# Kernel optimization log

Measured on AMD Instinct MI355X. Metric: run time of the kernel, lower is better.

## Reference

```python
import jax, jax.numpy as jnp
import numpy as np

N, E, IN, H = 100000, 400000, 128, 128
HEADS, HC = 4, 128  # GATConv(heads=4, out_channels=128, concat=False)
EPS = 1e-5


def setup_inputs() -> dict:
    key = jax.random.key(0)
    ks = jax.random.split(key, 16)
    rn = lambda i, shape, s=0.05: jax.random.normal(ks[i], shape, jnp.float32) * s
    return {
        "x": jax.random.normal(ks[0], (N, IN), jnp.float32),
        "edge_index": jax.random.randint(ks[1], (2, E), 0, N),
        # SAGEConv1: lin_l (aggregated neighbors, with bias) + lin_r (root)
        "Wl1": rn(2, (IN, H)), "Wr1": rn(3, (IN, H)), "b1": jnp.zeros((H,)),
        "g1": jnp.ones((H,)), "be1": jnp.zeros((H,)),
        # GATConv: shared lin, per-head attention vectors, bias (concat=False -> [HC])
        "Wg": rn(4, (H, HEADS * HC)), "att_s": rn(5, (HEADS, HC)), "att_d": rn(6, (HEADS, HC)), "bg": jnp.zeros((HC,)),
        "g2": jnp.ones((H,)), "be2": jnp.zeros((H,)),
        # SAGEConv3: hidden -> hidden//2
        "Wl3": rn(7, (H, H // 2)), "Wr3": rn(8, (H, H // 2)), "b3": jnp.zeros((H // 2,)),
        "g3": jnp.ones((H // 2,)), "be3": jnp.zeros((H // 2,)),
        # skip: in -> hidden//2
        "Wsk": rn(9, (IN, H // 2)), "bsk": jnp.zeros((H // 2,)),
        # classifier head: 64 -> 64 (BN+ReLU) -> 32 (ReLU) -> 2
        "Wc1": rn(10, (H // 2, 64)), "bc1": jnp.zeros((64,)),
        "gc": jnp.ones((64,)), "bec": jnp.zeros((64,)),
        "Wc2": rn(11, (64, 32)), "bc2": jnp.zeros((32,)),
        "Wc3": rn(12, (32, 2)), "bc3": jnp.zeros((2,)),
    }


def _bn(x, g, b):
    m = x.mean(0)
    v = x.var(0)
    return g * (x - m) * jax.lax.rsqrt(v + EPS) + b


def _sage(x, src, dst, Wl, Wr, b):
    # mean aggregation of neighbor features at dst, then lin_l(agg) + lin_r(x)
    agg = jax.ops.segment_sum(x[src], dst, num_segments=N)
    deg = jax.ops.segment_sum(jnp.ones((src.shape[0],), x.dtype), dst, num_segments=N)
    mean = agg / jnp.maximum(deg, 1.0)[:, None]
    return mean @ Wl + x @ Wr + b


def _gat(x, src, dst, Wg, att_s, att_d, bg):
    xh = (x @ Wg).reshape(N, HEADS, HC)          # [N,H,C]
    a_s = (xh * att_s).sum(-1)                    # [N,H]
    a_d = (xh * att_d).sum(-1)                    # [N,H]
    e = jax.nn.leaky_relu(a_s[src] + a_d[dst], 0.2)   # [E,H]
    emax = jax.lax.stop_gradient(jax.ops.segment_max(e, dst, num_segments=N))
    ee = jnp.exp(e - emax[dst])
    denom = jax.ops.segment_sum(ee, dst, num_segments=N)
    alpha = ee / jnp.maximum(denom, 1e-16)[dst]   # segment softmax over in-edges
    out = jax.ops.segment_sum(alpha[:, :, None] * xh[src], dst, num_segments=N)  # [N,H,C]
    return out.mean(1) + bg                       # concat=False -> mean over heads


def reference(x, edge_index, Wl1, Wr1, b1, g1, be1, Wg, att_s, att_d, bg, g2, be2,
              Wl3, Wr3, b3, g3, be3, Wsk, bsk, Wc1, bc1, gc, bec, Wc2, bc2, Wc3, bc3):
    src, dst = edge_index[0], edge_index[1]
    identity = x @ Wsk + bsk
    h = jax.nn.relu(_bn(_sage(x, src, dst, Wl1, Wr1, b1), g1, be1))
    h = jax.nn.relu(_bn(_gat(h, src, dst, Wg, att_s, att_d, bg), g2, be2))
    h = jax.nn.relu(_bn(_sage(h, src, dst, Wl3, Wr3, b3), g3, be3))
    emb = h + identity
    z = jax.nn.relu(_bn(emb @ Wc1 + bc1, gc, bec))
    z = jax.nn.relu(z @ Wc2 + bc2)
    return jax.nn.log_softmax(z @ Wc3 + bc3, axis=1)
```

## Files before the change

kernel.cpp:

```cpp
#include <hip/hip_runtime.h>
#include <hip/hip_bf16.h>
#include <cmath>


typedef short s16x8 __attribute__((ext_vector_type(8)));
typedef float f32x4 __attribute__((ext_vector_type(4)));

__device__ __forceinline__ float bf2f(unsigned short u) {
  return __uint_as_float((unsigned)u << 16);
}
__device__ __forceinline__ unsigned short f2bf(float f) {
  __hip_bfloat16 h = __float2bfloat16(f);
  return *reinterpret_cast<unsigned short*>(&h);
}

__global__ __launch_bounds__(256) void k_scan1(const int* __restrict__ cnt,
                                               int* __restrict__ bsum, int N) {
  int base = blockIdx.x << 10;
  int t = threadIdx.x;
  int s = 0;
  #pragma unroll
  for (int j = 0; j < 4; ++j) {
    int i = base + t * 4 + j;
    if (i < N) s += cnt[i];
  }
  __shared__ int red[256];
  red[t] = s;
  __syncthreads();
  for (int off = 128; off; off >>= 1) {
    if (t < off) red[t] += red[t + off];
    __syncthreads();
  }
  if (t == 0) bsum[blockIdx.x] = red[0];
}

__global__ __launch_bounds__(1024) void k_scan2(int* __restrict__ bsum, int nb) {
  __shared__ int sh[1024];
  int t = threadIdx.x;
  int v = (t < nb) ? bsum[t] : 0;
  sh[t] = v;
  __syncthreads();
  for (int off = 1; off < 1024; off <<= 1) {
    int u = (t >= off) ? sh[t - off] : 0;
    __syncthreads();
    sh[t] += u;
    __syncthreads();
  }
  if (t < nb) bsum[t] = sh[t] - v;
}

__global__ __launch_bounds__(256) void k_scan3(const int* __restrict__ cnt,
                                               const int* __restrict__ bsum,
                                               int* __restrict__ indptr,
                                               int* __restrict__ cursor, int N) {
  int base = blockIdx.x << 10;
  int t = threadIdx.x;
  int lane = t & 63, w = t >> 6;
  int i0 = base + t * 4;
  int v[4], s = 0;
  #pragma unroll
  for (int j = 0; j < 4; ++j) {
    int i = i0 + j;
    v[j] = (i < N) ? cnt[i] : 0;
    s += v[j];
  }
  int incl = s;
  #pragma unroll
  for (int off = 1; off < 64; off <<= 1) {
    int u = __shfl_up(incl, off);
    if (lane >= off) incl += u;
  }
  __shared__ int wsum[4];
  if (lane == 63) wsum[w] = incl;
  __syncthreads();
  int add = 0;
  for (int j = 0; j < w; ++j) add += wsum[j];
  int run = incl - s + add + bsum[blockIdx.x];
  #pragma unroll
  for (int j = 0; j < 4; ++j) {
    int i = i0 + j;
    if (i < N) {
      cursor[i] = run;
      run += v[j];
      indptr[i + 1] = run;
    }
  }
  if (blockIdx.x == 0 && t == 0) indptr[0] = 0;
}

__global__ void k_fill(const int* __restrict__ src, const int* __restrict__ dst,
                       int* __restrict__ cursor, int* __restrict__ csr_src, int E) {
  int e = blockIdx.x * blockDim.x + threadIdx.x;
  if (e >= E) return;
  int pos = atomicAdd(&cursor[dst[e]], 1);
  csr_src[pos] = src[e];
}

__global__ __launch_bounds__(256) void k_pre(
    const float* __restrict__ x, unsigned short* __restrict__ xbf, long n4,
    const int* __restrict__ dst, int* __restrict__ cnt, int E,
    int gC, int gE,
    const float* __restrict__ Wsk, const float* __restrict__ Wl1,
    const float* __restrict__ Wr1, const float* __restrict__ Wg,
    const float* __restrict__ Wl3, const float* __restrict__ Wr3,
    const float* __restrict__ Wc1, const float* __restrict__ Wc2,
    unsigned short* __restrict__ wt,
    const float* __restrict__ atts, const float* __restrict__ attd,
    float* __restrict__ attw) {
  int bx = blockIdx.x;
  if (bx < gC) {
    long t = (long)bx * 256 + threadIdx.x;
    if (t < n4) {
      float4 v = *reinterpret_cast<const float4*>(x + t * 4);
      ushort4 u;
      u.x = f2bf(v.x); u.y = f2bf(v.y); u.z = f2bf(v.z); u.w = f2bf(v.w);
      *reinterpret_cast<ushort4*>(xbf + t * 4) = u;
    }
    return;
  }
  bx -= gC;
  if (bx < gE) {
    int e = bx * 256 + threadIdx.x;
    if (e < E) atomicAdd(&cnt[dst[e]], 1);
    return;
  }
  bx -= gE;
  if (bx < 504) {
    int t = bx * 256 + threadIdx.x;
    if (t >= 129024) return;
    float v;
    if (t < 8192) {
      int c = t >> 7, k = t & 127;
      v = Wsk[k * 64 + c];
    } else if (t < 24576) {
      int r = t - 8192; int c = r >> 7, k = r & 127;
      v = Wl1[k * 128 + c];
    } else if (t < 40960) {
      int r = t - 24576; int c = r >> 7, k = r & 127;
      v = Wr1[k * 128 + c];
    } else if (t < 106496) {
      int r = t - 40960; int c = r >> 9; int q = r & 511; int h = q >> 7, k = q & 127;
      v = Wg[k * 512 + h * 128 + c];
    } else if (t < 114688) {
      int r = t - 106496; int c = r >> 7, k = r & 127;
      v = Wl3[k * 64 + c];
    } else if (t < 122880) {
      int r = t - 114688; int c = r >> 7, k = r & 127;
      v = Wr3[k * 64 + c];
    } else if (t < 126976) {
      int r = t - 122880; int c = r >> 6, k = r & 63;
      v = Wc1[k * 64 + c];
    } else {
      int r = t - 126976; int c = r >> 6, k = r & 63;
      v = Wc2[k * 32 + c];
    }
    wt[t] = f2bf(v);
    return;
  }
  bx -= 504;
  {
    int t = bx * 256 + threadIdx.x;
    if (t >= 1024) return;
    int k = t >> 3, j = t & 7, h = j & 3;
    const float* av = (j < 4 ? atts : attd) + h * 128;
    const float* wg = Wg + (size_t)k * 512 + h * 128;
    float s = 0.f;
    for (int c = 0; c < 128; ++c) s = fmaf(wg[c], av[c], s);
    attw[t] = s;
  }
}

__device__ __forceinline__ void gmean128_body(const unsigned short* __restrict__ X,
                                              const int* __restrict__ indptr,
                                              const int* __restrict__ csr,
                                              unsigned short* __restrict__ out,
                                              long wid, int lane) {
  int b = indptr[wid], en = indptr[wid + 1];
  float ax = 0.f, ay = 0.f;
  int i = b;
  for (; i + 3 < en; i += 4) {
    int s0 = csr[i], s1 = csr[i + 1], s2 = csr[i + 2], s3 = csr[i + 3];
    ushort2 u0 = *reinterpret_cast<const ushort2*>(X + ((size_t)s0 << 7) + (lane << 1));
    ushort2 u1 = *reinterpret_cast<const ushort2*>(X + ((size_t)s1 << 7) + (lane << 1));
    ushort2 u2 = *reinterpret_cast<const ushort2*>(X + ((size_t)s2 << 7) + (lane << 1));
    ushort2 u3 = *reinterpret_cast<const ushort2*>(X + ((size_t)s3 << 7) + (lane << 1));
    ax += bf2f(u0.x); ay += bf2f(u0.y);
    ax += bf2f(u1.x); ay += bf2f(u1.y);
    ax += bf2f(u2.x); ay += bf2f(u2.y);
    ax += bf2f(u3.x); ay += bf2f(u3.y);
  }
  for (; i < en; ++i) {
    int s = csr[i];
    ushort2 u = *reinterpret_cast<const ushort2*>(X + ((size_t)s << 7) + (lane << 1));
    ax += bf2f(u.x); ay += bf2f(u.y);
  }
  float inv = 1.0f / (float)max(en - b, 1);
  ax *= inv; ay *= inv;
  ushort2 o; o.x = f2bf(ax); o.y = f2bf(ay);
  *reinterpret_cast<ushort2*>(out + (wid << 7) + (lane << 1)) = o;
}

__global__ __launch_bounds__(256) void k_gmean64(const unsigned short* __restrict__ X,
                                                 const int* __restrict__ indptr,
                                                 const int* __restrict__ csr,
                                                 float* __restrict__ out, int N) {
  long wid = ((long)blockIdx.x * blockDim.x + threadIdx.x) >> 6;
  if (wid >= N) return;
  int lane = threadIdx.x & 63;
  int b = indptr[wid], en = indptr[wid + 1];
  float a = 0.f;
  int i = b;
  for (; i + 3 < en; i += 4) {
    int s0 = csr[i], s1 = csr[i + 1], s2 = csr[i + 2], s3 = csr[i + 3];
    unsigned short u0 = X[((size_t)s0 << 6) + lane];
    unsigned short u1 = X[((size_t)s1 << 6) + lane];
    unsigned short u2 = X[((size_t)s2 << 6) + lane];
    unsigned short u3 = X[((size_t)s3 << 6) + lane];
    a += bf2f(u0); a += bf2f(u1); a += bf2f(u2); a += bf2f(u3);
  }
  for (; i < en; ++i) {
    int s = csr[i];
    a += bf2f(X[((size_t)s << 6) + lane]);
  }
  out[(wid << 6) + lane] = a / (float)max(en - b, 1);
}

__global__ __launch_bounds__(256) void k_alpha(const int* __restrict__ indptr,
                                               const int* __restrict__ csr,
                                               const float* __restrict__ asad,
                                               float* __restrict__ alpha, int N) {
  long g = ((long)blockIdx.x * blockDim.x + threadIdx.x) >> 3;
  if (g >= N) return;
  int l8 = threadIdx.x & 7;
  int b = indptr[g], en = indptr[g + 1];
  float4 adv = *reinterpret_cast<const float4*>(asad + g * 8 + 4);
  float m[4] = {-INFINITY, -INFINITY, -INFINITY, -INFINITY};
  for (int i = b + l8; i < en; i += 8) {
    int s = csr[i];
    float4 a = *reinterpret_cast<const float4*>(asad + (size_t)s * 8);
    float e0 = a.x + adv.x, e1 = a.y + adv.y, e2 = a.z + adv.z, e3 = a.w + adv.w;
    e0 = e0 >= 0.f ? e0 : 0.2f * e0; e1 = e1 >= 0.f ? e1 : 0.2f * e1;
    e2 = e2 >= 0.f ? e2 : 0.2f * e2; e3 = e3 >= 0.f ? e3 : 0.2f * e3;
    m[0] = fmaxf(m[0], e0); m[1] = fmaxf(m[1], e1);
    m[2] = fmaxf(m[2], e2); m[3] = fmaxf(m[3], e3);
  }
  #pragma unroll
  for (int off = 1; off < 8; off <<= 1) {
    #pragma unroll
    for (int h = 0; h < 4; ++h) m[h] = fmaxf(m[h], __shfl_xor(m[h], off));
  }
  float den[4] = {0.f, 0.f, 0.f, 0.f};
  for (int i = b + l8; i < en; i += 8) {
    int s = csr[i];
    float4 a = *reinterpret_cast<const float4*>(asad + (size_t)s * 8);
    float e0 = a.x + adv.x, e1 = a.y + adv.y, e2 = a.z + adv.z, e3 = a.w + adv.w;
    e0 = e0 >= 0.f ? e0 : 0.2f * e0; e1 = e1 >= 0.f ? e1 : 0.2f * e1;
    e2 = e2 >= 0.f ? e2 : 0.2f * e2; e3 = e3 >= 0.f ? e3 : 0.2f * e3;
    float4 w;
    w.x = __expf(e0 - m[0]); w.y = __expf(e1 - m[1]);
    w.z = __expf(e2 - m[2]); w.w = __expf(e3 - m[3]);
    den[0] += w.x; den[1] += w.y; den[2] += w.z; den[3] += w.w;
    *reinterpret_cast<float4*>(alpha + (size_t)i * 4) = w;
  }
  #pragma unroll
  for (int off = 1; off < 8; off <<= 1) {
    #pragma unroll
    for (int h = 0; h < 4; ++h) den[h] += __shfl_xor(den[h], off);
  }
  float s0 = 0.25f / fmaxf(den[0], 1e-16f);
  float s1 = 0.25f / fmaxf(den[1], 1e-16f);
  float s2 = 0.25f / fmaxf(den[2], 1e-16f);
  float s3 = 0.25f / fmaxf(den[3], 1e-16f);
  for (int i = b + l8; i < en; i += 8) {
    float4 w = *reinterpret_cast<const float4*>(alpha + (size_t)i * 4);
    w.x *= s0; w.y *= s1; w.z *= s2; w.w *= s3;
    *reinterpret_cast<float4*>(alpha + (size_t)i * 4) = w;
  }
}

__global__ __launch_bounds__(256) void k_gath1(
    const unsigned short* __restrict__ h1, const int* __restrict__ indptr,
    const int* __restrict__ csr, const float* __restrict__ alpha,
    unsigned short* __restrict__ agg, int N) {
  long wid = ((long)blockIdx.x * blockDim.x + threadIdx.x) >> 6;
  if (wid >= N) return;
  int lane = threadIdx.x & 63;
  int b = indptr[wid], en = indptr[wid + 1];
  float a0x = 0.f, a0y = 0.f, a1x = 0.f, a1y = 0.f;
  float a2x = 0.f, a2y = 0.f, a3x = 0.f, a3y = 0.f;
  int i = b;
  for (; i + 3 < en; i += 4) {
    int s0 = csr[i], s1 = csr[i + 1], s2 = csr[i + 2], s3 = csr[i + 3];
    float4 A0 = *reinterpret_cast<const float4*>(alpha + (size_t)i * 4);
    float4 A1 = *reinterpret_cast<const float4*>(alpha + (size_t)(i + 1) * 4);
    float4 A2 = *reinterpret_cast<const float4*>(alpha + (size_t)(i + 2) * 4);
    float4 A3 = *reinterpret_cast<const float4*>(alpha + (size_t)(i + 3) * 4);
    ushort2 u0 = *reinterpret_cast<const ushort2*>(h1 + ((size_t)s0 << 7) + (lane << 1));
    ushort2 u1 = *reinterpret_cast<const ushort2*>(h1 + ((size_t)s1 << 7) + (lane << 1));
    ushort2 u2 = *reinterpret_cast<const ushort2*>(h1 + ((size_t)s2 << 7) + (lane << 1));
    ushort2 u3 = *reinterpret_cast<const ushort2*>(h1 + ((size_t)s3 << 7) + (lane << 1));
    float vx, vy;
    vx = bf2f(u0.x); vy = bf2f(u0.y);
    a0x = fmaf(A0.x, vx, a0x); a0y = fmaf(A0.x, vy, a0y);
    a1x = fmaf(A0.y, vx, a1x); a1y = fmaf(A0.y, vy, a1y);
    a2x = fmaf(A0.z, vx, a2x); a2y = fmaf(A0.z, vy, a2y);
    a3x = fmaf(A0.w, vx, a3x); a3y = fmaf(A0.w, vy, a3y);
    vx = bf2f(u1.x); vy = bf2f(u1.y);
    a0x = fmaf(A1.x, vx, a0x); a0y = fmaf(A1.x, vy, a0y);
    a1x = fmaf(A1.y, vx, a1x); a1y = fmaf(A1.y, vy, a1y);
    a2x = fmaf(A1.z, vx, a2x); a2y = fmaf(A1.z, vy, a2y);
    a3x = fmaf(A1.w, vx, a3x); a3y = fmaf(A1.w, vy, a3y);
    vx = bf2f(u2.x); vy = bf2f(u2.y);
    a0x = fmaf(A2.x, vx, a0x); a0y = fmaf(A2.x, vy, a0y);
    a1x = fmaf(A2.y, vx, a1x); a1y = fmaf(A2.y, vy, a1y);
    a2x = fmaf(A2.z, vx, a2x); a2y = fmaf(A2.z, vy, a2y);
    a3x = fmaf(A2.w, vx, a3x); a3y = fmaf(A2.w, vy, a3y);
    vx = bf2f(u3.x); vy = bf2f(u3.y);
    a0x = fmaf(A3.x, vx, a0x); a0y = fmaf(A3.x, vy, a0y);
    a1x = fmaf(A3.y, vx, a1x); a1y = fmaf(A3.y, vy, a1y);
    a2x = fmaf(A3.z, vx, a2x); a2y = fmaf(A3.z, vy, a2y);
    a3x = fmaf(A3.w, vx, a3x); a3y = fmaf(A3.w, vy, a3y);
  }
  for (; i < en; ++i) {
    int s = csr[i];
    float4 a = *reinterpret_cast<const float4*>(alpha + (size_t)i * 4);
    ushort2 u = *reinterpret_cast<const ushort2*>(h1 + ((size_t)s << 7) + (lane << 1));
    float vx = bf2f(u.x), vy = bf2f(u.y);
    a0x = fmaf(a.x, vx, a0x); a0y = fmaf(a.x, vy, a0y);
    a1x = fmaf(a.y, vx, a1x); a1y = fmaf(a.y, vy, a1y);
    a2x = fmaf(a.z, vx, a2x); a2y = fmaf(a.z, vy, a2y);
    a3x = fmaf(a.w, vx, a3x); a3y = fmaf(a.w, vy, a3y);
  }
  unsigned short* po = agg + ((size_t)wid << 9) + (lane << 1);
  ushort2 o;
  o.x = f2bf(a0x); o.y = f2bf(a0y); *reinterpret_cast<ushort2*>(po)       = o;
  o.x = f2bf(a1x); o.y = f2bf(a1y); *reinterpret_cast<ushort2*>(po + 128) = o;
  o.x = f2bf(a2x); o.y = f2bf(a2y); *reinterpret_cast<ushort2*>(po + 256) = o;
  o.x = f2bf(a3x); o.y = f2bf(a3y); *reinterpret_cast<ushort2*>(po + 384) = o;
}

template <int BNM>
__device__ __forceinline__ ushort4 load_a4(const void* A, int abf, int ldA,
                                           int gr, int col0,
                                           const float* sBN,
                                           const unsigned short* bnadd, int ldAdd) {
  if (BNM == 0) {
    if (abf) {
      return *reinterpret_cast<const ushort4*>(
          (const unsigned short*)A + (size_t)gr * ldA + col0);
    }
    float4 f = *reinterpret_cast<const float4*>(
        (const float*)A + (size_t)gr * ldA + col0);
    ushort4 u;
    u.x = f2bf(f.x); u.y = f2bf(f.y); u.z = f2bf(f.z); u.w = f2bf(f.w);
    return u;
  }
  float v[4];
  if (abf) {
    ushort4 u = *reinterpret_cast<const ushort4*>(
        (const unsigned short*)A + (size_t)gr * ldA + col0);
    v[0] = bf2f(u.x); v[1] = bf2f(u.y); v[2] = bf2f(u.z); v[3] = bf2f(u.w);
  } else {
    float4 f = *reinterpret_cast<const float4*>(
        (const float*)A + (size_t)gr * ldA + col0);
    v[0] = f.x; v[1] = f.y; v[2] = f.z; v[3] = f.w;
  }
  #pragma unroll
  for (int q = 0; q < 4; ++q) {
    int c = col0 + q;
    v[q] = fmaxf(fmaf(sBN[c], v[q], sBN[128 + c]), 0.f);
    if (BNM == 2) v[q] += bf2f(bnadd[(size_t)gr * ldAdd + c]);
  }
  ushort4 u;
  u.x = f2bf(v[0]); u.y = f2bf(v[1]); u.z = f2bf(v[2]); u.w = f2bf(v[3]);
  return u;
}

template <int CF, int BNM>
__device__ __forceinline__ void gemm_body(
    unsigned short* __restrict__ sA, unsigned short* __restrict__ sBt,
    int rowblk,
    const void* __restrict__ A1, int a1bf, int ldA1, int K1,
    const unsigned short* __restrict__ Wt1,
    const void* __restrict__ A2, int a2bf, int ldA2, int K2,
    const unsigned short* __restrict__ Wt2,
    const float* __restrict__ bias, const float* __restrict__ Cadd,
    void* __restrict__ Cout, int obf16,
    int Nrows, int ldC, int relu, float* __restrict__ spart,
    const float* __restrict__ bnst, const float* __restrict__ bng,
    const float* __restrict__ bnbt,
    const unsigned short* __restrict__ bnadd, int ldAdd) {
  constexpr int BN = CF * 32;
  const int tid = threadIdx.x;
  const int lane = tid & 63;
  const int w = tid >> 6;
  const int wr = (w >> 1) * 32;
  const int wc = (w & 1) * (CF * 16);
  const int lr = lane & 15;
  const int lk = (lane >> 4) << 3;
  const int row0 = rowblk * 128;
  const float invN = 1.0f / (float)Nrows;

  const float* bnp = nullptr;
  if constexpr (BNM > 0) {
    __shared__ float sBN[256];
    if (tid < 128 && tid < K1) {
      float m = bnst[tid] * invN;
      float var = bnst[128 + tid] * invN - m * m;
      float sc = bng[tid] * rsqrtf(var + 1e-5f);
      sBN[tid] = sc;
      sBN[128 + tid] = bnbt[tid] - sc * m;
    }
    __syncthreads();
    bnp = sBN;
  }

  f32x4 acc[2][CF];
  #pragma unroll
  for (int i = 0; i < 2; ++i)
    #pragma unroll
    for (int j = 0; j < CF; ++j) acc[i][j] = (f32x4){0.f, 0.f, 0.f, 0.f};

  const int kc = (tid << 2) & 63;
  const int r0 = (tid << 2) >> 6;
  ushort4 aR[4], bR[CF];

  for (int pass = 0; pass < 2; ++pass) {
    const void* A = pass ? A2 : A1;
    if (!A) break;
    const int abf = pass ? a2bf : a1bf;
    const int ldA = pass ? ldA2 : ldA1;
    const int K = pass ? K2 : K1;
    const unsigned short* Wt = pass ? Wt2 : Wt1;

    #pragma unroll
    for (int ii = 0; ii < 4; ++ii) {
      int gr = row0 + r0 + 32 * ii;
      aR[ii] = (gr < Nrows)
                   ? (pass ? load_a4<0>(A, abf, ldA, gr, kc, nullptr, nullptr, 0)
                           : load_a4<BNM>(A, abf, ldA, gr, kc, bnp, bnadd, ldAdd))
                   : make_ushort4(0, 0, 0, 0);
    }
    #pragma unroll
    for (int jj = 0; jj < CF; ++jj)
      bR[jj] = *reinterpret_cast<const ushort4*>(
          Wt + (size_t)(r0 + 32 * jj) * K + kc);

    for (int kb = 0; kb < K; kb += 64) {
      #pragma unroll
      for (int ii = 0; ii < 4; ++ii)
        *reinterpret_cast<ushort4*>(&sA[(r0 + 32 * ii) * 72 + kc]) = aR[ii];
      #pragma unroll
      for (int jj = 0; jj < CF; ++jj)
        *reinterpret_cast<ushort4*>(&sBt[(r0 + 32 * jj) * 72 + kc]) = bR[jj];
      __syncthreads();

      int kn = kb + 64;
      if (kn < K) {
        #pragma unroll
        for (int ii = 0; ii < 4; ++ii) {
          int gr = row0 + r0 + 32 * ii;
          aR[ii] = (gr < Nrows)
                       ? (pass ? load_a4<0>(A, abf, ldA, gr, kn + kc, nullptr, nullptr, 0)
                               : load_a4<BNM>(A, abf, ldA, gr, kn + kc, bnp, bnadd, ldAdd))
                       : make_ushort4(0, 0, 0, 0);
        }
        #pragma unroll
        for (int jj = 0; jj < CF; ++jj)
          bR[jj] = *reinterpret_cast<const ushort4*>(
              Wt + (size_t)(r0 + 32 * jj) * K + kn + kc);
      }

      #pragma unroll
      for (int ki = 0; ki < 2; ++ki) {
        int k0 = lk + ki * 32;
        s16x8 a0 = *reinterpret_cast<const s16x8*>(&sA[(wr + lr) * 72 + k0]);
        s16x8 a1 = *reinterpret_cast<const s16x8*>(&sA[(wr + lr + 16) * 72 + k0]);
        #pragma unroll
        for (int j = 0; j < CF; ++j) {
          s16x8 bj = *reinterpret_cast<const s16x8*>(&sBt[(wc + lr + 16 * j) * 72 + k0]);
          acc[0][j] = __builtin_amdgcn_mfma_f32_16x16x32_bf16(a0, bj, acc[0][j], 0, 0, 0);
          acc[1][j] = __builtin_amdgcn_mfma_f32_16x16x32_bf16(a1, bj, acc[1][j], 0, 0, 0);
        }
      }
      __syncthreads();
    }
  }

  const int rbase = (lane >> 4) << 2;
  float ps[CF], ps2[CF];
  #pragma unroll
  for (int j = 0; j < CF; ++j) { ps[j] = 0.f; ps2[j] = 0.f; }
  #pragma unroll
  for (int i = 0; i < 2; ++i) {
    int grow = row0 + wr + 16 * i + rbase;
    #pragma unroll
    for (int j = 0; j < CF; ++j) {
      int col = wc + 16 * j + lr;
      float bv = bias ? bias[col] : 0.f;
      #pragma unroll
      for (int r = 0; r < 4; ++r) {
        if (grow + r >= Nrows) continue;
        float v = acc[i][j][r] + bv;
        if (Cadd) v += Cadd[(size_t)(grow + r) * ldC + col];
        if (relu) v = fmaxf(v, 0.f);
        ps[j] += v;
        ps2[j] = fmaf(v, v, ps2[j]);
        if (obf16)
          ((unsigned short*)Cout)[(size_t)(grow + r) * ldC + col] = f2bf(v);
        else
          ((float*)Cout)[(size_t)(grow + r) * ldC + col] = v;
      }
    }
  }

  if (spart) {
    #pragma unroll
    for (int j = 0; j < CF; ++j) {
      float a = ps[j], b2 = ps2[j];
      a += __shfl_xor(a, 16); b2 += __shfl_xor(b2, 16);
      a += __shfl_xor(a, 32); b2 += __shfl_xor(b2, 32);
      ps[j] = a; ps2[j] = b2;
    }
    float* sred = reinterpret_cast<float*>(sA);
    if (lane < 16) {
      #pragma unroll
      for (int j = 0; j < CF; ++j) {
        sred[(w * CF + j) * 16 + lane] = ps[j];
        sred[1024 + (w * CF + j) * 16 + lane] = ps2[j];
      }
    }
    __syncthreads();
    int c = tid;
    if (c < BN) {
      int j = (c >= CF * 16) ? (c >> 4) - CF : (c >> 4);
      int wpar = (c >= CF * 16) ? 1 : 0;
      int lr2 = c & 15;
      float s = 0.f, s2 = 0.f;
      for (int ww = wpar; ww < 8; ww += 2) {
        s += sred[(ww * CF + j) * 16 + lr2];
        s2 += sred[1024 + (ww * CF + j) * 16 + lr2];
      }
      spart[(size_t)c * 1024 + rowblk] = s;
      spart[131072 + (size_t)c * 1024 + rowblk] = s2;
    }
  }
}

template <int CF, int BNM>
__global__ __launch_bounds__(512, 4) void k_mgemm(
    const void* __restrict__ A1, int a1bf, int ldA1, int K1,
    const unsigned short* __restrict__ Wt1,
    const void* __restrict__ A2, int a2bf, int ldA2, int K2,
    const unsigned short* __restrict__ Wt2,
    const float* __restrict__ bias, const float* __restrict__ Cadd,
    void* __restrict__ Cout, int obf16,
    int Nrows, int ldC, int relu, float* __restrict__ spart,
    const float* __restrict__ bnst, const float* __restrict__ bng,
    const float* __restrict__ bnbt,
    const unsigned short* __restrict__ bnadd, int ldAdd) {
  __shared__ unsigned short smem[128 * 72 + CF * 32 * 72];
  gemm_body<CF, BNM>(smem, smem + 128 * 72, blockIdx.x,
                     A1, a1bf, ldA1, K1, Wt1, A2, a2bf, ldA2, K2, Wt2,
                     bias, Cadd, Cout, obf16, Nrows, ldC, relu, spart,
                     bnst, bng, bnbt, bnadd, ldAdd);
}

__global__ __launch_bounds__(512, 4) void k_sage1(
    const unsigned short* __restrict__ xbf, const unsigned short* __restrict__ WtSk,
    const float* __restrict__ bsk, unsigned short* __restrict__ idbf,
    const int* __restrict__ indptr, const int* __restrict__ csr,
    unsigned short* __restrict__ mean1bf, int N, int gWsk) {
  if ((int)blockIdx.x < gWsk) {
    __shared__ unsigned short smem[128 * 72 + 64 * 72];
    gemm_body<2, 0>(smem, smem + 128 * 72, blockIdx.x,
                    xbf, 1, 128, 128, WtSk, nullptr, 0, 0, 0, nullptr,
                    bsk, nullptr, idbf, 1, N, 64, 0, nullptr,
                    nullptr, nullptr, nullptr, nullptr, 0);
  } else {
    long wid = (long)(blockIdx.x - gWsk) * 8 + (threadIdx.x >> 6);
    if (wid < N) gmean128_body(xbf, indptr, csr, mean1bf, wid, threadIdx.x & 63);
  }
}

__global__ __launch_bounds__(512, 4) void k_sage3(
    const unsigned short* __restrict__ h2bf,
    const unsigned short* __restrict__ WtL3, const unsigned short* __restrict__ WtR3,
    unsigned short* __restrict__ yl3, float* __restrict__ h3p,
    const float* __restrict__ b3,
    const float* __restrict__ st2, const float* __restrict__ g2,
    const float* __restrict__ be2, int N, int gHalf) {
  __shared__ unsigned short smem[128 * 72 + 64 * 72];
  if ((int)blockIdx.x < gHalf) {
    gemm_body<2, 1>(smem, smem + 128 * 72, blockIdx.x,
                    h2bf, 1, 128, 128, WtL3, nullptr, 0, 0, 0, nullptr,
                    nullptr, nullptr, yl3, 1, N, 64, 0, nullptr,
                    st2, g2, be2, nullptr, 0);
  } else {
    gemm_body<2, 1>(smem, smem + 128 * 72, blockIdx.x - gHalf,
                    h2bf, 1, 128, 128, WtR3, nullptr, 0, 0, 0, nullptr,
                    b3, nullptr, h3p, 0, N, 64, 0, nullptr,
                    st2, g2, be2, nullptr, 0);
  }
}

__global__ __launch_bounds__(256) void k_addstats(
    float* __restrict__ X, const float* __restrict__ add, long n,
    float* __restrict__ spart) {
  int c = threadIdx.x & 63;
  float s = 0.f, s2 = 0.f;
  for (long i = (long)blockIdx.x * 256 + threadIdx.x; i < n; i += 262144) {
    float v = X[i] + add[i];
    X[i] = v;
    s += v;
    s2 = fmaf(v, v, s2);
  }
  __shared__ float r1[256], r2[256];
  r1[threadIdx.x] = s; r2[threadIdx.x] = s2;
  __syncthreads();
  if (threadIdx.x < 64) {
    float a = r1[threadIdx.x] + r1[threadIdx.x + 64] + r1[threadIdx.x + 128] +
              r1[threadIdx.x + 192];
    float b = r2[threadIdx.x] + r2[threadIdx.x + 64] + r2[threadIdx.x + 128] +
              r2[threadIdx.x + 192];
    spart[(size_t)c * 1024 + blockIdx.x] = a;
    spart[131072 + (size_t)c * 1024 + blockIdx.x] = b;
  }
}

__global__ __launch_bounds__(256) void k_statred(const float* __restrict__ part,
                                                 float* __restrict__ st, int nb) {
  int c = blockIdx.x;
  int t = threadIdx.x;
  float s = 0.f, s2 = 0.f;
  for (int b = t; b < nb; b += 256) {
    s += part[(size_t)c * 1024 + b];
    s2 += part[131072 + (size_t)c * 1024 + b];
  }
  __shared__ float r1[256], r2[256];
  r1[t] = s; r2[t] = s2;
  __syncthreads();
  for (int off = 128; off; off >>= 1) {
    if (t < off) { r1[t] += r1[t + off]; r2[t] += r2[t + off]; }
    __syncthreads();
  }
  if (t == 0) { st[c] = r1[0]; st[128 + c] = r2[0]; }
}

__global__ void k_bnatt(unsigned short* __restrict__ X, const float* __restrict__ stats,
                        const float* __restrict__ g, const float* __restrict__ b,
                        const float* __restrict__ attw,
                        float* __restrict__ asad, int Nrows) {
  int lane = threadIdx.x & 63;
  int c0 = 2 * lane, c1 = 2 * lane + 1;
  float invN = 1.0f / (float)Nrows;
  float m0 = stats[c0] * invN;
  float v0 = stats[128 + c0] * invN - m0 * m0;
  float sc0 = g[c0] * rsqrtf(v0 + 1e-5f);
  float t0 = b[c0] - sc0 * m0;
  float m1 = stats[c1] * invN;
  float v1 = stats[128 + c1] * invN - m1 * m1;
  float sc1 = g[c1] * rsqrtf(v1 + 1e-5f);
  float t1 = b[c1] - sc1 * m1;
  float cA[8], cB[8];
  #pragma unroll
  for (int j = 0; j < 8; ++j) {
    cA[j] = attw[c0 * 8 + j];
    cB[j] = attw[c1 * 8 + j];
  }
  long wid = ((long)blockIdx.x * blockDim.x + threadIdx.x) >> 6;
  long nw = ((long)gridDim.x * blockDim.x) >> 6;
  for (long n = wid; n < Nrows; n += nw) {
    unsigned short* p = X + (n << 7) + (lane << 1);
    ushort2 u = *reinterpret_cast<const ushort2*>(p);
    float y0 = fmaxf(fmaf(sc0, bf2f(u.x), t0), 0.f);
    float y1 = fmaxf(fmaf(sc1, bf2f(u.y), t1), 0.f);
    ushort2 o; o.x = f2bf(y0); o.y = f2bf(y1);
    *reinterpret_cast<ushort2*>(p) = o;
    float a[8];
    #pragma unroll
    for (int j = 0; j < 8; ++j) a[j] = y0 * cA[j] + y1 * cB[j];
    float b4[4];
    #pragma unroll
    for (int j = 0; j < 4; ++j) {
      float keepv = (lane & 32) ? a[j + 4] : a[j];
      float sendv = (lane & 32) ? a[j] : a[j + 4];
      b4[j] = keepv + __shfl_xor(sendv, 32);
    }
    float c2[2];
    #pragma unroll
    for (int j = 0; j < 2; ++j) {
      float keepv = (lane & 16) ? b4[j + 2] : b4[j];
      float sendv = (lane & 16) ? b4[j] : b4[j + 2];
      c2[j] = keepv + __shfl_xor(sendv, 16);
    }
    float keepv = (lane & 8) ? c2[1] : c2[0];
    float sendv = (lane & 8) ? c2[0] : c2[1];
    float d = keepv + __shfl_xor(sendv, 8);
    d += __shfl_xor(d, 4);
    d += __shfl_xor(d, 2);
    d += __shfl_xor(d, 1);
    if ((lane & 7) == 0) asad[n * 8 + (lane >> 3)] = d;
  }
}

__global__ void k_final(const float* __restrict__ z2, const float* __restrict__ W,
                        const float* __restrict__ b, float* __restrict__ out, int Nrows) {
  int n = blockIdx.x * blockDim.x + threadIdx.x;
  if (n >= Nrows) return;
  float l0 = b[0], l1 = b[1];
  const float* z = z2 + (size_t)n * 32;
  #pragma unroll
  for (int k = 0; k < 32; ++k) {
    float v = z[k];
    l0 = fmaf(v, W[2 * k], l0);
    l1 = fmaf(v, W[2 * k + 1], l1);
  }
  float m = fmaxf(l0, l1);
  float lse = m + logf(expf(l0 - m) + expf(l1 - m));
  out[2 * n] = l0 - lse;
  out[2 * n + 1] = l1 - lse;
}

extern "C" void kernel_launch(void* const* d_in, const int* in_sizes, int n_in,
                              void* d_out, int out_size, void* d_ws, size_t ws_size,
                              hipStream_t stream) {
  const float* x    = (const float*)d_in[0];
  const int*   ei   = (const int*)  d_in[1];
  const float* Wl1  = (const float*)d_in[2];
  const float* Wr1  = (const float*)d_in[3];
  const float* b1   = (const float*)d_in[4];
  const float* g1   = (const float*)d_in[5];
  const float* be1  = (const float*)d_in[6];
  const float* Wg   = (const float*)d_in[7];
  const float* atts = (const float*)d_in[8];
  const float* attd = (const float*)d_in[9];
  const float* g2   = (const float*)d_in[11];
  const float* be2  = (const float*)d_in[12];
  const float* Wl3  = (const float*)d_in[13];
  const float* Wr3  = (const float*)d_in[14];
  const float* b3   = (const float*)d_in[15];
  const float* g3   = (const float*)d_in[16];
  const float* be3  = (const float*)d_in[17];
  const float* Wsk  = (const float*)d_in[18];
  const float* bsk  = (const float*)d_in[19];
  const float* Wc1  = (const float*)d_in[20];
  const float* bc1  = (const float*)d_in[21];
  const float* gc   = (const float*)d_in[22];
  const float* bec  = (const float*)d_in[23];
  const float* Wc2  = (const float*)d_in[24];
  const float* bc2  = (const float*)d_in[25];
  const float* Wc3  = (const float*)d_in[26];
  const float* bc3  = (const float*)d_in[27];
  (void)n_in; (void)out_size; (void)ws_size;

  const int N = in_sizes[0] / 128;
  const int E = in_sizes[1] / 2;
  const int* src = ei;
  const int* dst = ei + E;

  auto al4 = [](size_t w) { return (w + 3) & ~(size_t)3; };
  float* ws = (float*)d_ws;
  size_t o = 0;
  int* cnt      = (int*)(ws + o); o += al4((size_t)N);
  int* indptr   = (int*)(ws + o); o += al4((size_t)N + 1);
  int* cursor   = (int*)(ws + o); o += al4((size_t)N);
  int* csr_src  = (int*)(ws + o); o += al4((size_t)E);
  int* bsum     = (int*)(ws + o); o += 1024;
  unsigned short* idbf = (unsigned short*)(ws + o); o += al4((size_t)N * 32);
  float* stats  = ws + o; o += 1024;
  float* spart  = ws + o; o += 262144;
  float* attw   = ws + o; o += 1024;
  float* asad   = ws + o; o += al4((size_t)N * 8);
  float* alpha  = ws + o; o += al4((size_t)E * 4);
  unsigned short* wt = (unsigned short*)(ws + o); o += 64512 + 64;
  float* bufA   = ws + o; o += (size_t)N * 128;
  float* hb1    = ws + o; o += (size_t)N * 64;
  float* hB     = ws + o; o += (size_t)N * 128;
  unsigned short* agg = (unsigned short*)(ws + o); o += (size_t)N * 256;

  unsigned short* xbf     = (unsigned short*)bufA;
  unsigned short* mean1bf = (unsigned short*)(bufA + (size_t)N * 64);
  unsigned short* h1bf    = (unsigned short*)hb1;
  unsigned short* h2bf    = (unsigned short*)bufA;
  unsigned short* yl3     = agg;
  float* mean3f           = (float*)agg + (size_t)N * 32;
  float* h3 = hB;
  float* z1 = bufA + (size_t)N * 64;
  float* z2 = hB + (size_t)N * 64;

  unsigned short* WtSk = wt;
  unsigned short* WtL1 = WtSk + 8192;
  unsigned short* WtR1 = WtL1 + 16384;
  unsigned short* WtG2 = WtR1 + 16384;
  unsigned short* WtL3 = WtG2 + 65536;
  unsigned short* WtR3 = WtL3 + 8192;
  unsigned short* WtC1 = WtR3 + 8192;
  unsigned short* WtC2 = WtC1 + 4096;

  float* st1 = stats, *st2 = stats + 256, *st3 = stats + 512, *st4 = stats + 768;

  dim3 blk(256);
  dim3 blk512(512);
  int gE     = (E + 255) / 256;
  int gN128  = (N + 127) / 128;
  int gSC    = (N + 1023) / 1024;
  int gW     = (int)(((long)N * 64 + 255) / 256);
  int gA     = (int)(((long)N * 8 + 255) / 256);
  int gC     = (int)(((long)N * 32 + 255) / 256);
  int gGM8   = (N + 7) / 8;

  hipMemsetAsync(cnt, 0, (size_t)N * 4, stream);

  k_pre<<<gC + gE + 504 + 4, blk, 0, stream>>>(
      x, xbf, (long)N * 32, dst, cnt, E, gC, gE,
      Wsk, Wl1, Wr1, Wg, Wl3, Wr3, Wc1, Wc2, wt, atts, attd, attw);
  k_scan1<<<gSC, blk, 0, stream>>>(cnt, bsum, N);
  k_scan2<<<1, 1024, 0, stream>>>(bsum, gSC);
  k_scan3<<<gSC, blk, 0, stream>>>(cnt, bsum, indptr, cursor, N);
  k_fill<<<gE, blk, 0, stream>>>(src, dst, cursor, csr_src, E);

  k_sage1<<<gN128 + gGM8, blk512, 0, stream>>>(
      xbf, WtSk, bsk, idbf, indptr, csr_src, mean1bf, N, gN128);
  k_mgemm<4, 0><<<dim3(gN128, 1), blk512, 0, stream>>>(
      mean1bf, 1, 128, 128, WtL1, xbf, 1, 128, 128, WtR1,
      b1, nullptr, h1bf, 1, N, 128, 0, spart,
      nullptr, nullptr, nullptr, nullptr, 0);
  k_statred<<<128, blk, 0, stream>>>(spart, st1, gN128);

  k_bnatt<<<2048, blk, 0, stream>>>(h1bf, st1, g1, be1, attw, asad, N);
  k_alpha<<<gA, blk, 0, stream>>>(indptr, csr_src, asad, alpha, N);
  k_gath1<<<gW, blk, 0, stream>>>(h1bf, indptr, csr_src, alpha, agg, N);
  k_mgemm<4, 0><<<dim3(gN128, 1), blk512, 0, stream>>>(
      agg, 1, 512, 512, WtG2, nullptr, 0, 0, 0, nullptr,
      nullptr, nullptr, h2bf, 1, N, 128, 0, spart,
      nullptr, nullptr, nullptr, nullptr, 0);
  k_statred<<<128, blk, 0, stream>>>(spart, st2, gN128);

  k_sage3<<<2 * gN128, blk512, 0, stream>>>(
      h2bf, WtL3, WtR3, yl3, h3, b3, st2, g2, be2, N, gN128);
  k_gmean64<<<gW, blk, 0, stream>>>(yl3, indptr, csr_src, mean3f, N);
  k_addstats<<<1024, blk, 0, stream>>>(h3, mean3f, (long)N * 64, spart);
  k_statred<<<64, blk, 0, stream>>>(spart, st3, 1024);

  k_mgemm<2, 2><<<dim3(gN128, 1), blk512, 0, stream>>>(
      h3, 0, 64, 64, WtC1, nullptr, 0, 0, 0, nullptr,
      bc1, nullptr, z1, 0, N, 64, 0, spart,
      st3, g3, be3, idbf, 64);
  k_statred<<<64, blk, 0, stream>>>(spart, st4, gN128);
  k_mgemm<1, 1><<<dim3(gN128, 1), blk512, 0, stream>>>(
      z1, 0, 64, 64, WtC2, nullptr, 0, 0, 0, nullptr,
      bc2, nullptr, z2, 0, N, 32, 1, nullptr,
      st4, gc, bec, nullptr, 0);
  k_final<<<(N + 255) / 256, blk, 0, stream>>>(z2, Wc3, bc3, (float*)d_out, N);
}
```

Before: 447.0 us.

## Split GAT gather into halves and overlap second half with first-half GEMM

After: 453.0 us. Within noise of the previous version (+1.3%).

```diff
diff --git a/kernel.cpp b/kernel.cpp
--- a/kernel.cpp
+++ b/kernel.cpp
@@ -278,13 +278,10 @@
   }
 }
 
-__global__ __launch_bounds__(256) void k_gath1(
+__device__ __forceinline__ void gath1_body(
     const unsigned short* __restrict__ h1, const int* __restrict__ indptr,
     const int* __restrict__ csr, const float* __restrict__ alpha,
-    unsigned short* __restrict__ agg, int N) {
-  long wid = ((long)blockIdx.x * blockDim.x + threadIdx.x) >> 6;
-  if (wid >= N) return;
-  int lane = threadIdx.x & 63;
+    unsigned short* __restrict__ agg, long wid, int lane) {
   int b = indptr[wid], en = indptr[wid + 1];
   float a0x = 0.f, a0y = 0.f, a1x = 0.f, a1y = 0.f;
   float a2x = 0.f, a2y = 0.f, a3x = 0.f, a3y = 0.f;
@@ -339,6 +336,15 @@
   o.x = f2bf(a3x); o.y = f2bf(a3y); *reinterpret_cast<ushort2*>(po + 384) = o;
 }
 
+__global__ __launch_bounds__(256) void k_gath1r(
+    const unsigned short* __restrict__ h1, const int* __restrict__ indptr,
+    const int* __restrict__ csr, const float* __restrict__ alpha,
+    unsigned short* __restrict__ agg, long nEnd) {
+  long wid = ((long)blockIdx.x * blockDim.x + threadIdx.x) >> 6;
+  if (wid >= nEnd) return;
+  gath1_body(h1, indptr, csr, alpha, agg, wid, threadIdx.x & 63);
+}
+
 template <int BNM>
 __device__ __forceinline__ ushort4 load_a4(const void* A, int abf, int ldA,
                                            int gr, int col0,
@@ -558,9 +564,9 @@
     int Nrows, int ldC, int relu, float* __restrict__ spart,
     const float* __restrict__ bnst, const float* __restrict__ bng,
     const float* __restrict__ bnbt,
-    const unsigned short* __restrict__ bnadd, int ldAdd) {
+    const unsigned short* __restrict__ bnadd, int ldAdd, int rowOff) {
   __shared__ unsigned short smem[128 * 72 + CF * 32 * 72];
-  gemm_body<CF, BNM>(smem, smem + 128 * 72, blockIdx.x,
+  gemm_body<CF, BNM>(smem, smem + 128 * 72, blockIdx.x + rowOff,
                      A1, a1bf, ldA1, K1, Wt1, A2, a2bf, ldA2, K2, Wt2,
                      bias, Cadd, Cout, obf16, Nrows, ldC, relu, spart,
                      bnst, bng, bnbt, bnadd, ldAdd);
@@ -580,6 +586,24 @@
   } else {
     long wid = (long)(blockIdx.x - gWsk) * 8 + (threadIdx.x >> 6);
     if (wid < N) gmean128_body(xbf, indptr, csr, mean1bf, wid, threadIdx.x & 63);
+  }
+}
+
+__global__ __launch_bounds__(512, 4) void k_gatmix(
+    const unsigned short* __restrict__ h1, const int* __restrict__ indptr,
+    const int* __restrict__ csr, const float* __restrict__ alpha,
+    unsigned short* __restrict__ agg, const unsigned short* __restrict__ WtG2,
+    unsigned short* __restrict__ h2bf, float* __restrict__ spart,
+    int N, int gGemm, long nBase) {
+  if ((int)blockIdx.x < gGemm) {
+    __shared__ unsigned short smem[128 * 72 + 128 * 72];
+    gemm_body<4, 0>(smem, smem + 128 * 72, blockIdx.x,
+                    agg, 1, 512, 512, WtG2, nullptr, 0, 0, 0, nullptr,
+                    nullptr, nullptr, h2bf, 1, N, 128, 0, spart,
+                    nullptr, nullptr, nullptr, nullptr, 0);
+  } else {
+    long wid = nBase + (long)(blockIdx.x - gGemm) * 8 + (threadIdx.x >> 6);
+    if (wid < N) gath1_body(h1, indptr, csr, alpha, agg, wid, threadIdx.x & 63);
   }
 }
 
@@ -786,7 +810,7 @@
   unsigned short* yl3     = agg;
   float* mean3f           = (float*)agg + (size_t)N * 32;
   float* h3 = hB;
-  float* z1 = bufA + (size_t)N * 64;
+  unsigned short* z1bf    = agg;
   float* z2 = hB + (size_t)N * 64;
 
   unsigned short* WtSk = wt;
@@ -810,6 +834,11 @@
   int gC     = (int)(((long)N * 32 + 255) / 256);
   int gGM8   = (N + 7) / 8;
 
+  int gHalf  = gN128 / 2;
+  long nBase = (long)gHalf * 128;
+  int gGa0   = (int)((nBase * 64 + 255) / 256);
+  int gGa1   = (int)((N - nBase + 7) / 8);
+
   hipMemsetAsync(cnt, 0, (size_t)N * 4, stream);
 
   k_pre<<<gC + gE + 504 + 4, blk, 0, stream>>>(
@@ -825,16 +854,18 @@
   k_mgemm<4, 0><<<dim3(gN128, 1), blk512, 0, stream>>>(
       mean1bf, 1, 128, 128, WtL1, xbf, 1, 128, 128, WtR1,
       b1, nullptr, h1bf, 1, N, 128, 0, spart,
-      nullptr, nullptr, nullptr, nullptr, 0);
+      nullptr, nullptr, nullptr, nullptr, 0, 0);
   k_statred<<<128, blk, 0, stream>>>(spart, st1, gN128);
 
   k_bnatt<<<2048, blk, 0, stream>>>(h1bf, st1, g1, be1, attw, asad, N);
   k_alpha<<<gA, blk, 0, stream>>>(indptr, csr_src, asad, alpha, N);
-  k_gath1<<<gW, blk, 0, stream>>>(h1bf, indptr, csr_src, alpha, agg, N);
-  k_mgemm<4, 0><<<dim3(gN128, 1), blk512, 0, stream>>>(
+  k_gath1r<<<gGa0, blk, 0, stream>>>(h1bf, indptr, csr_src, alpha, agg, nBase);
+  k_gatmix<<<gHalf + gGa1, blk512, 0, stream>>>(
+      h1bf, indptr, csr_src, alpha, agg, WtG2, h2bf, spart, N, gHalf, nBase);
+  k_mgemm<4, 0><<<dim3(gN128 - gHalf, 1), blk512, 0, stream>>>(
       agg, 1, 512, 512, WtG2, nullptr, 0, 0, 0, nullptr,
       nullptr, nullptr, h2bf, 1, N, 128, 0, spart,
-      nullptr, nullptr, nullptr, nullptr, 0);
+      nullptr, nullptr, nullptr, nullptr, 0, gHalf);
   k_statred<<<128, blk, 0, stream>>>(spart, st2, gN128);
 
   k_sage3<<<2 * gN128, blk512, 0, stream>>>(
@@ -845,12 +876,12 @@
 
   k_mgemm<2, 2><<<dim3(gN128, 1), blk512, 0, stream>>>(
       h3, 0, 64, 64, WtC1, nullptr, 0, 0, 0, nullptr,
-      bc1, nullptr, z1, 0, N, 64, 0, spart,
-      st3, g3, be3, idbf, 64);
+      bc1, nullptr, z1bf, 1, N, 64, 0, spart,
+      st3, g3, be3, idbf, 64, 0);
   k_statred<<<64, blk, 0, stream>>>(spart, st4, gN128);
   k_mgemm<1, 1><<<dim3(gN128, 1), blk512, 0, stream>>>(
-      z1, 0, 64, 64, WtC2, nullptr, 0, 0, 0, nullptr,
+      z1bf, 1, 64, 64, WtC2, nullptr, 0, 0, 0, nullptr,
       bc2, nullptr, z2, 0, N, 32, 1, nullptr,
-      st4, gc, bec, nullptr, 0);
+      st4, gc, bec, nullptr, 0, 0);
   k_final<<<(N + 255) / 256, blk, 0, stream>>>(z2, Wc3, bc3, (float*)d_out, N);
 }
```

## Use direct global-to-LDS loads with XOR swizzle for bf16 GEMM tiles; bf16 z1

Applied to the files above, without the earlier changes.

New measurement: 426.7 us. -4.5%, faster.

```diff
diff --git a/kernel.cpp b/kernel.cpp
--- a/kernel.cpp
+++ b/kernel.cpp
@@ -5,6 +5,7 @@
 
 typedef short s16x8 __attribute__((ext_vector_type(8)));
 typedef float f32x4 __attribute__((ext_vector_type(4)));
+typedef unsigned int u32;
 
 __device__ __forceinline__ float bf2f(unsigned short u) {
   return __uint_as_float((unsigned)u << 16);
@@ -12,6 +13,12 @@
 __device__ __forceinline__ unsigned short f2bf(float f) {
   __hip_bfloat16 h = __float2bfloat16(f);
   return *reinterpret_cast<unsigned short*>(&h);
+}
+
+__device__ __forceinline__ void gload16(const void* g, void* l) {
+  __builtin_amdgcn_global_load_lds(
+      (const __attribute__((address_space(1))) u32*)g,
+      (__attribute__((address_space(3))) u32*)l, 16, 0, 0);
 }
 
 __global__ __launch_bounds__(256) void k_scan1(const int* __restrict__ cnt,
@@ -391,6 +398,7 @@
     const float* __restrict__ bnbt,
     const unsigned short* __restrict__ bnadd, int ldAdd) {
   constexpr int BN = CF * 32;
+  constexpr int LDW = (BNM == 0) ? 64 : 72;
   const int tid = threadIdx.x;
   const int lane = tid & 63;
   const int w = tid >> 6;
@@ -421,69 +429,116 @@
     #pragma unroll
     for (int j = 0; j < CF; ++j) acc[i][j] = (f32x4){0.f, 0.f, 0.f, 0.f};
 
-  const int kc = (tid << 2) & 63;
-  const int r0 = (tid << 2) >> 6;
-  ushort4 aR[4], bR[CF];
-
-  for (int pass = 0; pass < 2; ++pass) {
-    const void* A = pass ? A2 : A1;
-    if (!A) break;
-    const int abf = pass ? a2bf : a1bf;
-    const int ldA = pass ? ldA2 : ldA1;
-    const int K = pass ? K2 : K1;
-    const unsigned short* Wt = pass ? Wt2 : Wt1;
-
-    #pragma unroll
-    for (int ii = 0; ii < 4; ++ii) {
-      int gr = row0 + r0 + 32 * ii;
-      aR[ii] = (gr < Nrows)
-                   ? (pass ? load_a4<0>(A, abf, ldA, gr, kc, nullptr, nullptr, 0)
-                           : load_a4<BNM>(A, abf, ldA, gr, kc, bnp, bnadd, ldAdd))
-                   : make_ushort4(0, 0, 0, 0);
-    }
-    #pragma unroll
-    for (int jj = 0; jj < CF; ++jj)
-      bR[jj] = *reinterpret_cast<const ushort4*>(
-          Wt + (size_t)(r0 + 32 * jj) * K + kc);
-
-    for (int kb = 0; kb < K; kb += 64) {
+  auto lidx = [&](int row, int k0) -> int {
+    if constexpr (BNM == 0) return row * 64 + (k0 ^ ((row & 7) << 3));
+    else                    return row * 72 + k0;
+  };
+
+  if constexpr (BNM == 0) {
+    const int lhi = lane >> 3;
+    const int bsw = (((lane & 7) ^ lhi) << 3);
+    for (int pass = 0; pass < 2; ++pass) {
+      const void* A = pass ? A2 : A1;
+      if (!A) break;
+      const int ldA = pass ? ldA2 : ldA1;
+      const int K = pass ? K2 : K1;
+      const unsigned short* Wt = pass ? Wt2 : Wt1;
+      const unsigned short* Au = (const unsigned short*)A;
+
+      for (int kb = 0; kb < K; kb += 64) {
+        #pragma unroll
+        for (int s = 0; s < 2; ++s) {
+          int seg = w + s * 8;
+          int gr = row0 + seg * 8 + lhi;
+          if (gr >= Nrows) gr = Nrows - 1;
+          gload16(Au + (size_t)gr * ldA + kb + bsw, sA + seg * 512);
+        }
+        for (int seg = w; seg < (BN >> 3); seg += 8) {
+          int r = seg * 8 + lhi;
+          gload16(Wt + (size_t)r * K + kb + bsw, sBt + seg * 512);
+        }
+        __syncthreads();
+
+        #pragma unroll
+        for (int ki = 0; ki < 2; ++ki) {
+          int k0 = lk + ki * 32;
+          s16x8 a0 = *reinterpret_cast<const s16x8*>(&sA[lidx(wr + lr, k0)]);
+          s16x8 a1 = *reinterpret_cast<const s16x8*>(&sA[lidx(wr + lr + 16, k0)]);
+          #pragma unroll
+          for (int j = 0; j < CF; ++j) {
+            s16x8 bj = *reinterpret_cast<const s16x8*>(&sBt[lidx(wc + lr + 16 * j, k0)]);
+            acc[0][j] = __builtin_amdgcn_mfma_f32_16x16x32_bf16(a0, bj, acc[0][j], 0, 0, 0);
+            acc[1][j] = __builtin_amdgcn_mfma_f32_16x16x32_bf16(a1, bj, acc[1][j], 0, 0, 0);
+          }
+        }
+        __syncthreads();
+      }
+    }
+  } else {
+    const int kc = (tid << 2) & 63;
+    const int r0 = (tid << 2) >> 6;
+    ushort4 aR[4], bR[CF];
+
+    for (int pass = 0; pass < 2; ++pass) {
+      const void* A = pass ? A2 : A1;
+      if (!A) break;
+      const int abf = pass ? a2bf : a1bf;
+      const int ldA = pass ? ldA2 : ldA1;
+      const int K = pass ? K2 : K1;
+      const unsigned short* Wt = pass ? Wt2 : Wt1;
+
       #pragma unroll
-      for (int ii = 0; ii < 4; ++ii)
-        *reinterpret_cast<ushort4*>(&sA[(r0 + 32 * ii) * 72 + kc]) = aR[ii];
+      for (int ii = 0; ii < 4; ++ii) {
+        int gr = row0 + r0 + 32 * ii;
+        aR[ii] = (gr < Nrows)
+                     ? (pass ? load_a4<0>(A, abf, ldA, gr, kc, nullptr, nullptr, 0)
+                             : load_a4<BNM>(A, abf, ldA, gr, kc, bnp, bnadd, ldAdd))
+                     : make_ushort4(0, 0, 0, 0);
+      }
       #pragma unroll
       for (int jj = 0; jj < CF; ++jj)
-        *reinterpret_cast<ushort4*>(&sBt[(r0 + 32 * jj) * 72 + kc]) = bR[jj];
-      __syncthreads();
-
-      int kn = kb + 64;
-      if (kn < K) {
+        bR[jj] = *reinterpret_cast<const ushort4*>(
+            Wt + (size_t)(r0 + 32 * jj) * K + kc);
+
+      for (int kb = 0; kb < K; kb += 64) {
         #pragma unroll
-        for (int ii = 0; ii < 4; ++ii) {
-          int gr = row0 + r0 + 32 * ii;
-          aR[ii] = (gr < Nrows)
-                       ? (pass ? load_a4<0>(A, abf, ldA, gr, kn + kc, nullptr, nullptr, 0)
-                               : load_a4<BNM>(A, abf, ldA, gr, kn + kc, bnp, bnadd, ldAdd))
-                       : make_ushort4(0, 0, 0, 0);
-        }
+        for (int ii = 0; ii < 4; ++ii)
+          *reinterpret_cast<ushort4*>(&sA[(r0 + 32 * ii) * 72 + kc]) = aR[ii];
         #pragma unroll
         for (int jj = 0; jj < CF; ++jj)
-          bR[jj] = *reinterpret_cast<const ushort4*>(
-              Wt + (size_t)(r0 + 32 * jj) * K + kn + kc);
+          *reinterpret_cast<ushort4*>(&sBt[(r0 + 32 * jj) * 72 + kc]) = bR[jj];
+        __syncthreads();
+
+        int kn = kb + 64;
+        if (kn < K) {
+          #pragma unroll
+          for (int ii = 0; ii < 4; ++ii) {
+            int gr = row0 + r0 + 32 * ii;
+            aR[ii] = (gr < Nrows)
+                         ? (pass ? load_a4<0>(A, abf, ldA, gr, kn + kc, nullptr, nullptr, 0)
+                                 : load_a4<BNM>(A, abf, ldA, gr, kn + kc, bnp, bnadd, ldAdd))
+                         : make_ushort4(0, 0, 0, 0);
+          }
+          #pragma unroll
+          for (int jj = 0; jj < CF; ++jj)
+            bR[jj] = *reinterpret_cast<const ushort4*>(
+                Wt + (size_t)(r0 + 32 * jj) * K + kn + kc);
+        }
+
+        #pragma unroll
+        for (int ki = 0; ki < 2; ++ki) {
+          int k0 = lk + ki * 32;
+          s16x8 a0 = *reinterpret_cast<const s16x8*>(&sA[(wr + lr) * 72 + k0]);
+          s16x8 a1 = *reinterpret_cast<const s16x8*>(&sA[(wr + lr + 16) * 72 + k0]);
+          #pragma unroll
+          for (int j = 0; j < CF; ++j) {
+            s16x8 bj = *reinterpret_cast<const s16x8*>(&sBt[(wc + lr + 16 * j) * 72 + k0]);
+            acc[0][j] = __builtin_amdgcn_mfma_f32_16x16x32_bf16(a0, bj, acc[0][j], 0, 0, 0);
+            acc[1][j] = __builtin_amdgcn_mfma_f32_16x16x32_bf16(a1, bj, acc[1][j], 0, 0, 0);
+          }
+        }
+        __syncthreads();
       }
-
-      #pragma unroll
-      for (int ki = 0; ki < 2; ++ki) {
-        int k0 = lk + ki * 32;
-        s16x8 a0 = *reinterpret_cast<const s16x8*>(&sA[(wr + lr) * 72 + k0]);
-        s16x8 a1 = *reinterpret_cast<const s16x8*>(&sA[(wr + lr + 16) * 72 + k0]);
-        #pragma unroll
-        for (int j = 0; j < CF; ++j) {
-          s16x8 bj = *reinterpret_cast<const s16x8*>(&sBt[(wc + lr + 16 * j) * 72 + k0]);
-          acc[0][j] = __builtin_amdgcn_mfma_f32_16x16x32_bf16(a0, bj, acc[0][j], 0, 0, 0);
-          acc[1][j] = __builtin_amdgcn_mfma_f32_16x16x32_bf16(a1, bj, acc[1][j], 0, 0, 0);
-        }
-      }
-      __syncthreads();
     }
   }
 
@@ -559,8 +614,9 @@
     const float* __restrict__ bnst, const float* __restrict__ bng,
     const float* __restrict__ bnbt,
     const unsigned short* __restrict__ bnadd, int ldAdd) {
-  __shared__ unsigned short smem[128 * 72 + CF * 32 * 72];
-  gemm_body<CF, BNM>(smem, smem + 128 * 72, blockIdx.x,
+  constexpr int LDW = (BNM == 0) ? 64 : 72;
+  __shared__ alignas(16) unsigned short smem[(128 + CF * 32) * LDW];
+  gemm_body<CF, BNM>(smem, smem + 128 * LDW, blockIdx.x,
                      A1, a1bf, ldA1, K1, Wt1, A2, a2bf, ldA2, K2, Wt2,
                      bias, Cadd, Cout, obf16, Nrows, ldC, relu, spart,
                      bnst, bng, bnbt, bnadd, ldAdd);
@@ -572,8 +628,8 @@
     const int* __restrict__ indptr, const int* __restrict__ csr,
     unsigned short* __restrict__ mean1bf, int N, int gWsk) {
   if ((int)blockIdx.x < gWsk) {
-    __shared__ unsigned short smem[128 * 72 + 64 * 72];
-    gemm_body<2, 0>(smem, smem + 128 * 72, blockIdx.x,
+    __shared__ alignas(16) unsigned short smem[(128 + 64) * 64];
+    gemm_body<2, 0>(smem, smem + 128 * 64, blockIdx.x,
                     xbf, 1, 128, 128, WtSk, nullptr, 0, 0, 0, nullptr,
                     bsk, nullptr, idbf, 1, N, 64, 0, nullptr,
                     nullptr, nullptr, nullptr, nullptr, 0);
@@ -590,7 +646,7 @@
     const float* __restrict__ b3,
     const float* __restrict__ st2, const float* __restrict__ g2,
     const float* __restrict__ be2, int N, int gHalf) {
-  __shared__ unsigned short smem[128 * 72 + 64 * 72];
+  __shared__ alignas(16) unsigned short smem[(128 + 64) * 72];
   if ((int)blockIdx.x < gHalf) {
     gemm_body<2, 1>(smem, smem + 128 * 72, blockIdx.x,
                     h2bf, 1, 128, 128, WtL3, nullptr, 0, 0, 0, nullptr,
@@ -786,7 +842,7 @@
   unsigned short* yl3     = agg;
   float* mean3f           = (float*)agg + (size_t)N * 32;
   float* h3 = hB;
-  float* z1 = bufA + (size_t)N * 64;
+  unsigned short* z1bf    = agg;
   float* z2 = hB + (size_t)N * 64;
 
   unsigned short* WtSk = wt;
@@ -845,11 +901,11 @@
 
   k_mgemm<2, 2><<<dim3(gN128, 1), blk512, 0, stream>>>(
       h3, 0, 64, 64, WtC1, nullptr, 0, 0, 0, nullptr,
-      bc1, nullptr, z1, 0, N, 64, 0, spart,
+      bc1, nullptr, z1bf, 1, N, 64, 0, spart,
       st3, g3, be3, idbf, 64);
   k_statred<<<64, blk, 0, stream>>>(spart, st4, gN128);
   k_mgemm<1, 1><<<dim3(gN128, 1), blk512, 0, stream>>>(
-      z1, 0, 64, 64, WtC2, nullptr, 0, 0, 0, nullptr,
+      z1bf, 1, 64, 64, WtC2, nullptr, 0, 0, 0, nullptr,
       bc2, nullptr, z2, 0, N, 32, 1, nullptr,
       st4, gc, bec, nullptr, 0);
   k_final<<<(N + 255) / 256, blk, 0, stream>>>(z2, Wc3, bc3, (float*)d_out, N);
```
